# Kernel tuning notes

Hardware: AMD Instinct MI355X
Metric: run time of the kernel (lower is better)

Reference implementation:

```python
import jax, jax.numpy as jnp
import numpy as np

BATCH_SIZE = 2048
TEMPERATURE = 0.5
EPS = 1e-8  # torch CosineSimilarity eps


def setup_inputs() -> dict:
    key = jax.random.key(0)
    k1, k2 = jax.random.split(key)
    d = 512
    z_i = jax.random.normal(k1, (BATCH_SIZE, d), dtype=jnp.float32)
    z_j = jax.random.normal(k2, (BATCH_SIZE, d), dtype=jnp.float32)
    return {"z_i": z_i, "z_j": z_j}


def reference(z_i, z_j):
    B = BATCH_SIZE
    n = 2 * B
    z = jnp.concatenate([z_i, z_j], axis=0)              # [n, d]
    # cosine similarity via normalize + GEMM (same math as broadcasted CosineSimilarity)
    norms = jnp.maximum(jnp.linalg.norm(z, axis=1, keepdims=True), EPS)
    zn = z / norms                                       # [n, d]
    S = zn @ zn.T                                        # [n, n]
    # drop diagonal: row i keeps columns j != i, in order (matches sim[~eye].view(n, n-1))
    cols = jnp.arange(n - 1)[None, :]                    # [1, n-1]
    rows = jnp.arange(n)[:, None]                        # [n, 1]
    idx = cols + (cols >= rows)                          # skip diagonal
    off_diag = jnp.take_along_axis(S, idx, axis=1)       # [n, n-1]
    # positive pair: pos_pairs = cat(z_j, z_i) -> partner index (i + B) mod n
    pos = jnp.take_along_axis(S, ((rows[:, 0] + B) % n)[:, None], axis=1)  # [n, 1]
    logits = jnp.concatenate([pos, off_diag], axis=1) / TEMPERATURE        # [n, n]
    # cross-entropy with label 0, reduction='sum', then / n  == mean over rows
    loss = jnp.mean(jax.nn.logsumexp(logits, axis=1) - logits[:, 0])
    return loss
```

## Files before the change

kernel.cpp:

```cpp
#include <hip/hip_runtime.h>
#include <hip/hip_bf16.h>

#define N_TOT 4096
#define D     512
#define BHALF 2048

#define EXP2_SCALE 2.8853900817779268f
#define E2 7.3890560989306495f

typedef __attribute__((ext_vector_type(4))) float floatx4;

__global__ void normalize_kernel(const float* __restrict__ z_i,
                                 const float* __restrict__ z_j,
                                 unsigned char* __restrict__ zn,
                                 float* __restrict__ rowsum) {
    const int wave = threadIdx.x >> 6, lane = threadIdx.x & 63;
    const int row = blockIdx.x * 4 + wave;
    const float* src = (row < BHALF) ? (z_i + (size_t)row * D)
                                     : (z_j + (size_t)(row - BHALF) * D);
    if (lane == 0) rowsum[row] = 0.0f;
    float4 v0 = ((const float4*)src)[lane];
    float4 v1 = ((const float4*)src)[lane + 64];
    float ss = v0.x*v0.x + v0.y*v0.y + v0.z*v0.z + v0.w*v0.w
             + v1.x*v1.x + v1.y*v1.y + v1.z*v1.z + v1.w*v1.w;
    #pragma unroll
    for (int off = 32; off > 0; off >>= 1) ss += __shfl_xor(ss, off);
    float inv = 1.0f / fmaxf(sqrtf(ss), 1e-8f);
    int w0 = __builtin_amdgcn_cvt_pk_fp8_f32(v0.x * inv, v0.y * inv, 0, false);
    w0     = __builtin_amdgcn_cvt_pk_fp8_f32(v0.z * inv, v0.w * inv, w0, true);
    int w1 = __builtin_amdgcn_cvt_pk_fp8_f32(v1.x * inv, v1.y * inv, 0, false);
    w1     = __builtin_amdgcn_cvt_pk_fp8_f32(v1.z * inv, v1.w * inv, w1, true);
    int* dst = (int*)(zn + (size_t)row * D);
    dst[lane]      = w0;
    dst[lane + 64] = w1;
}

__launch_bounds__(256)
__global__ void gemm_fused(const unsigned char* __restrict__ zn,
                           float* __restrict__ rowsum,
                           float* __restrict__ spos) {
    int b = blockIdx.x, bi = 0, rowlen = 32;
    while (b >= rowlen) { b -= rowlen; rowlen--; bi++; }
    const int bj = bi + b;
    const int i0 = bi * 128;
    const int j0 = bj * 128;

    const int t = threadIdx.x;
    const int lane = t & 63, wave = t >> 6;
    const int wm = wave & 1, wn = wave >> 1;
    const int quad = lane >> 4, l16 = lane & 15;

    const unsigned char* pA = zn + (size_t)(i0 + wm*64 + l16) * D + quad*8;
    const unsigned char* pB = zn + (size_t)(j0 + wn*64 + l16) * D + quad*8;

    floatx4 acc[4][4] = {};
    long a0[4], b0[4], a1[4], b1[4];

    #pragma unroll
    for (int tm = 0; tm < 4; ++tm) a0[tm] = *(const long*)(pA + tm*16*D);
    #pragma unroll
    for (int tn = 0; tn < 4; ++tn) b0[tn] = *(const long*)(pB + tn*16*D);

    #pragma unroll
    for (int kt = 0; kt < 16; ++kt) {
        if (kt < 15) {
            const int ko = (kt + 1) * 32;
            #pragma unroll
            for (int tm = 0; tm < 4; ++tm)
                a1[tm] = *(const long*)(pA + tm*16*D + ko);
            #pragma unroll
            for (int tn = 0; tn < 4; ++tn)
                b1[tn] = *(const long*)(pB + tn*16*D + ko);
        }
        #pragma unroll
        for (int tm = 0; tm < 4; ++tm)
            #pragma unroll
            for (int tn = 0; tn < 4; ++tn)
                acc[tm][tn] = __builtin_amdgcn_mfma_f32_16x16x32_fp8_fp8(
                    a0[tm], b0[tn], acc[tm][tn], 0, 0, 0);
        #pragma unroll
        for (int i = 0; i < 4; ++i) { a0[i] = a1[i]; b0[i] = b1[i]; }
    }

    float cs[4] = {0.f, 0.f, 0.f, 0.f};
    #pragma unroll
    for (int tm = 0; tm < 4; ++tm) {
        float rs[4] = {0.f, 0.f, 0.f, 0.f};
        #pragma unroll
        for (int tn = 0; tn < 4; ++tn)
            #pragma unroll
            for (int r = 0; r < 4; ++r) {
                float e = exp2f(acc[tm][tn][r] * EXP2_SCALE);
                rs[r] += e;
                cs[tn] += e;
            }
        #pragma unroll
        for (int r = 0; r < 4; ++r) {
            float v = rs[r];
            v += __shfl_xor(v, 1);
            v += __shfl_xor(v, 2);
            v += __shfl_xor(v, 4);
            v += __shfl_xor(v, 8);
            if (l16 == 0) {
                int gi = i0 + wm*64 + tm*16 + quad*4 + r;
                atomicAdd(&rowsum[gi], v);
            }
        }
    }
    if (bi != bj) {
        #pragma unroll
        for (int tn = 0; tn < 4; ++tn) {
            float v = cs[tn];
            v += __shfl_xor(v, 16);
            v += __shfl_xor(v, 32);
            if (quad == 0) {
                int gj = j0 + wn*64 + tn*16 + l16;
                atomicAdd(&rowsum[gj], v);
            }
        }
    }
    if (bj == bi + 16) {
        #pragma unroll
        for (int tm = 0; tm < 4; ++tm)
            #pragma unroll
            for (int tn = 0; tn < 4; ++tn)
                #pragma unroll
                for (int r = 0; r < 4; ++r) {
                    int li = wm*64 + tm*16 + quad*4 + r;
                    int lj = wn*64 + tn*16 + l16;
                    if (li == lj) {
                        float s = acc[tm][tn][r];
                        spos[i0 + li]         = s;
                        spos[i0 + li + BHALF] = s;
                    }
                }
    }
}

__global__ void finalize_kernel(const float* __restrict__ rowsum,
                                const float* __restrict__ spos,
                                float* __restrict__ out) {
    int t = threadIdx.x;
    float acc = 0.f;
    for (int i = t; i < N_TOT; i += 1024) {
        float sp = spos[i];
        float denom = rowsum[i] - E2 + exp2f(sp * EXP2_SCALE);
        acc += __logf(denom) - 2.0f * sp;
    }
    #pragma unroll
    for (int off = 32; off > 0; off >>= 1) acc += __shfl_xor(acc, off);
    __shared__ float red[16];
    if ((t & 63) == 0) red[t >> 6] = acc;
    __syncthreads();
    if (t == 0) {
        float s = 0.f;
        #pragma unroll
        for (int w = 0; w < 16; ++w) s += red[w];
        out[0] = s / (float)N_TOT;
    }
}

extern "C" void kernel_launch(void* const* d_in, const int* in_sizes, int n_in,
                              void* d_out, int out_size, void* d_ws, size_t ws_size,
                              hipStream_t stream) {
    const float* z_i = (const float*)d_in[0];
    const float* z_j = (const float*)d_in[1];
    float* out = (float*)d_out;

    char* ws = (char*)d_ws;
    unsigned char* zn = (unsigned char*)ws;
    float* rowsum = (float*)(ws + (size_t)N_TOT * D);
    float* spos   = rowsum + N_TOT;

    normalize_kernel<<<N_TOT / 4, 256, 0, stream>>>(z_i, z_j, zn, rowsum);
    gemm_fused<<<(32 * 33) / 2, 256, 0, stream>>>(zn, rowsum, spos);
    finalize_kernel<<<1, 1024, 0, stream>>>(rowsum, spos, out);
}
```

Measured before the change: 110.3 us.

## Compute full similarity matrix without symmetry and replace atomics with partial-sum slots

The GEMM no longer exploits symmetry. Each of 512 blocks computes a 128-row strip against 256 columns, so the full 4096x4096 matrix is computed. Row sums of the exponentials go to 32 per-slot partial buffers with plain stores instead of atomicAdd, and the finalize kernel reduces those slots, which also removes the need to zero rowsum in normalize. This roughly doubles the MFMA and exp work in exchange for removing atomic contention, column-sum shuffles and the triangular index loop, and it gives more uniform blocks.

```diff
diff --git a/kernel.cpp b/kernel.cpp
--- a/kernel.cpp
+++ b/kernel.cpp
@@ -12,13 +12,11 @@
 
 __global__ void normalize_kernel(const float* __restrict__ z_i,
                                  const float* __restrict__ z_j,
-                                 unsigned char* __restrict__ zn,
-                                 float* __restrict__ rowsum) {
+                                 unsigned char* __restrict__ zn) {
     const int wave = threadIdx.x >> 6, lane = threadIdx.x & 63;
     const int row = blockIdx.x * 4 + wave;
     const float* src = (row < BHALF) ? (z_i + (size_t)row * D)
                                      : (z_j + (size_t)(row - BHALF) * D);
-    if (lane == 0) rowsum[row] = 0.0f;
     float4 v0 = ((const float4*)src)[lane];
     float4 v1 = ((const float4*)src)[lane + 64];
     float ss = v0.x*v0.x + v0.y*v0.y + v0.z*v0.z + v0.w*v0.w
@@ -37,13 +35,11 @@
 
 __launch_bounds__(256)
 __global__ void gemm_fused(const unsigned char* __restrict__ zn,
-                           float* __restrict__ rowsum,
+                           float* __restrict__ rowsum_part,
                            float* __restrict__ spos) {
-    int b = blockIdx.x, bi = 0, rowlen = 32;
-    while (b >= rowlen) { b -= rowlen; rowlen--; bi++; }
-    const int bj = bi + b;
-    const int i0 = bi * 128;
-    const int j0 = bj * 128;
+    const int s = blockIdx.x >> 4;
+    const int c = blockIdx.x & 15;
+    const int i0 = s * 128;
 
     const int t = threadIdx.x;
     const int lane = t & 63, wave = t >> 6;
@@ -51,100 +47,99 @@
     const int quad = lane >> 4, l16 = lane & 15;
 
     const unsigned char* pA = zn + (size_t)(i0 + wm*64 + l16) * D + quad*8;
-    const unsigned char* pB = zn + (size_t)(j0 + wn*64 + l16) * D + quad*8;
 
-    floatx4 acc[4][4] = {};
-    long a0[4], b0[4], a1[4], b1[4];
+    float rs[4][4];
+    #pragma unroll
+    for (int tm = 0; tm < 4; ++tm)
+        #pragma unroll
+        for (int r = 0; r < 4; ++r) rs[tm][r] = 0.f;
 
     #pragma unroll
-    for (int tm = 0; tm < 4; ++tm) a0[tm] = *(const long*)(pA + tm*16*D);
-    #pragma unroll
-    for (int tn = 0; tn < 4; ++tn) b0[tn] = *(const long*)(pB + tn*16*D);
+    for (int jt = 0; jt < 2; ++jt) {
+        const int j0 = c * 256 + jt * 128;
+        const unsigned char* pB = zn + (size_t)(j0 + wn*64 + l16) * D + quad*8;
 
-    #pragma unroll
-    for (int kt = 0; kt < 16; ++kt) {
-        if (kt < 15) {
-            const int ko = (kt + 1) * 32;
+        floatx4 acc[4][4] = {};
+        long a0[4], b0[4], a1[4], b1[4];
+        #pragma unroll
+        for (int tm = 0; tm < 4; ++tm) a0[tm] = *(const long*)(pA + tm*16*D);
+        #pragma unroll
+        for (int tn = 0; tn < 4; ++tn) b0[tn] = *(const long*)(pB + tn*16*D);
+
+        #pragma unroll
+        for (int kt = 0; kt < 16; ++kt) {
+            if (kt < 15) {
+                const int ko = (kt + 1) * 32;
+                #pragma unroll
+                for (int tm = 0; tm < 4; ++tm)
+                    a1[tm] = *(const long*)(pA + tm*16*D + ko);
+                #pragma unroll
+                for (int tn = 0; tn < 4; ++tn)
+                    b1[tn] = *(const long*)(pB + tn*16*D + ko);
+            }
             #pragma unroll
             for (int tm = 0; tm < 4; ++tm)
-                a1[tm] = *(const long*)(pA + tm*16*D + ko);
+                #pragma unroll
+                for (int tn = 0; tn < 4; ++tn)
+                    acc[tm][tn] = __builtin_amdgcn_mfma_f32_16x16x32_fp8_fp8(
+                        a0[tm], b0[tn], acc[tm][tn], 0, 0, 0);
             #pragma unroll
-            for (int tn = 0; tn < 4; ++tn)
-                b1[tn] = *(const long*)(pB + tn*16*D + ko);
+            for (int i = 0; i < 4; ++i) { a0[i] = a1[i]; b0[i] = b1[i]; }
         }
+
         #pragma unroll
         for (int tm = 0; tm < 4; ++tm)
             #pragma unroll
             for (int tn = 0; tn < 4; ++tn)
-                acc[tm][tn] = __builtin_amdgcn_mfma_f32_16x16x32_fp8_fp8(
-                    a0[tm], b0[tn], acc[tm][tn], 0, 0, 0);
-        #pragma unroll
-        for (int i = 0; i < 4; ++i) { a0[i] = a1[i]; b0[i] = b1[i]; }
+                #pragma unroll
+                for (int r = 0; r < 4; ++r)
+                    rs[tm][r] += exp2f(acc[tm][tn][r] * EXP2_SCALE);
+
+        if (j0 == (i0 ^ BHALF)) {
+            #pragma unroll
+            for (int tm = 0; tm < 4; ++tm)
+                #pragma unroll
+                for (int tn = 0; tn < 4; ++tn)
+                    #pragma unroll
+                    for (int r = 0; r < 4; ++r) {
+                        int li = wm*64 + tm*16 + quad*4 + r;
+                        int lj = wn*64 + tn*16 + l16;
+                        if (li == lj) spos[i0 + li] = acc[tm][tn][r];
+                    }
+        }
     }
 
-    float cs[4] = {0.f, 0.f, 0.f, 0.f};
+    const int slot = c * 2 + wn;
     #pragma unroll
-    for (int tm = 0; tm < 4; ++tm) {
-        float rs[4] = {0.f, 0.f, 0.f, 0.f};
-        #pragma unroll
-        for (int tn = 0; tn < 4; ++tn)
-            #pragma unroll
-            for (int r = 0; r < 4; ++r) {
-                float e = exp2f(acc[tm][tn][r] * EXP2_SCALE);
-                rs[r] += e;
-                cs[tn] += e;
-            }
+    for (int tm = 0; tm < 4; ++tm)
         #pragma unroll
         for (int r = 0; r < 4; ++r) {
-            float v = rs[r];
+            float v = rs[tm][r];
             v += __shfl_xor(v, 1);
             v += __shfl_xor(v, 2);
             v += __shfl_xor(v, 4);
             v += __shfl_xor(v, 8);
             if (l16 == 0) {
                 int gi = i0 + wm*64 + tm*16 + quad*4 + r;
-                atomicAdd(&rowsum[gi], v);
+                rowsum_part[slot * N_TOT + gi] = v;
             }
         }
-    }
-    if (bi != bj) {
-        #pragma unroll
-        for (int tn = 0; tn < 4; ++tn) {
-            float v = cs[tn];
-            v += __shfl_xor(v, 16);
-            v += __shfl_xor(v, 32);
-            if (quad == 0) {
-                int gj = j0 + wn*64 + tn*16 + l16;
-                atomicAdd(&rowsum[gj], v);
-            }
-        }
-    }
-    if (bj == bi + 16) {
-        #pragma unroll
-        for (int tm = 0; tm < 4; ++tm)
-            #pragma unroll
-            for (int tn = 0; tn < 4; ++tn)
-                #pragma unroll
-                for (int r = 0; r < 4; ++r) {
-                    int li = wm*64 + tm*16 + quad*4 + r;
-                    int lj = wn*64 + tn*16 + l16;
-                    if (li == lj) {
-                        float s = acc[tm][tn][r];
-                        spos[i0 + li]         = s;
-                        spos[i0 + li + BHALF] = s;
-                    }
-                }
-    }
 }
 
-__global__ void finalize_kernel(const float* __restrict__ rowsum,
+__global__ void finalize_kernel(const float* __restrict__ rowsum_part,
                                 const float* __restrict__ spos,
                                 float* __restrict__ out) {
     int t = threadIdx.x;
     float acc = 0.f;
-    for (int i = t; i < N_TOT; i += 1024) {
-        float sp = spos[i];
-        float denom = rowsum[i] - E2 + exp2f(sp * EXP2_SCALE);
+    #pragma unroll
+    for (int rr = 0; rr < 4; ++rr) {
+        int row = t + rr * 1024;
+        float sum = 0.f;
+        #pragma unroll
+        for (int slot = 0; slot < 32; ++slot)
+            sum += rowsum_part[slot * N_TOT + row];
+        float sp = spos[row];
+        float denom = sum - E2 + exp2f(sp * EXP2_SCALE);
         acc += __logf(denom) - 2.0f * sp;
     }
     #pragma unroll
@@ -153,10 +148,10 @@
     if ((t & 63) == 0) red[t >> 6] = acc;
     __syncthreads();
     if (t == 0) {
-        float s = 0.f;
+        float ssum = 0.f;
         #pragma unroll
-        for (int w = 0; w < 16; ++w) s += red[w];
-        out[0] = s / (float)N_TOT;
+        for (int w = 0; w < 16; ++w) ssum += red[w];
+        out[0] = ssum / (float)N_TOT;
     }
 }
 
@@ -168,11 +163,11 @@
     float* out = (float*)d_out;
 
     char* ws = (char*)d_ws;
-    unsigned char* zn = (unsigned char*)ws;
-    float* rowsum = (float*)(ws + (size_t)N_TOT * D);
-    float* spos   = rowsum + N_TOT;
+    unsigned char* zn  = (unsigned char*)ws;
+    float* rowsum_part = (float*)(ws + (size_t)N_TOT * D);
+    float* spos        = rowsum_part + 32 * N_TOT;
 
-    normalize_kernel<<<N_TOT / 4, 256, 0, stream>>>(z_i, z_j, zn, rowsum);
-    gemm_fused<<<(32 * 33) / 2, 256, 0, stream>>>(zn, rowsum, spos);
-    finalize_kernel<<<1, 1024, 0, stream>>>(rowsum, spos, out);
+    normalize_kernel<<<N_TOT / 4, 256, 0, stream>>>(z_i, z_j, zn);
+    gemm_fused<<<512, 256, 0, stream>>>(zn, rowsum_part, spos);
+    finalize_kernel<<<1, 1024, 0, stream>>>(rowsum_part, spos, out);
 }
```

Result: slower. 157.8 us (+43.0%).
